# Performance work log

Measured on AMD Instinct MI355X. Metric: run time of the kernel, lower is better.

Reference implementation:

```python
import jax, jax.numpy as jnp
import numpy as np

N = 4096  # query nodes
L = 4096  # source nodes
C = 512   # in_channels == out_channels (required by the original code path)
H = 8     # num_heads
DK = C // H  # 64


def setup_inputs() -> dict:
    key = jax.random.key(0)
    ks = jax.random.split(key, 12)
    s = 1.0 / np.sqrt(C)
    return {
        "query_input": jax.random.normal(ks[0], (N, C), jnp.float32),
        "source_input": jax.random.normal(ks[1], (L, C), jnp.float32),
        # outer value projection (TransConvLayerGAT.Wv): C -> C
        "Wv_out_w": jax.random.uniform(ks[2], (C, C), jnp.float32, -s, s),
        "Wv_out_b": jax.random.uniform(ks[3], (C,), jnp.float32, -s, s),
        # attention projections
        "Wq_w": jax.random.uniform(ks[4], (C, H * DK), jnp.float32, -s, s),
        "Wq_b": jax.random.uniform(ks[5], (H * DK,), jnp.float32, -s, s),
        "Wk_w": jax.random.uniform(ks[6], (C, H * DK), jnp.float32, -s, s),
        "Wk_b": jax.random.uniform(ks[7], (H * DK,), jnp.float32, -s, s),
        # attention value projection: C -> H * out_channels
        "Wv_attn_w": jax.random.uniform(ks[8], (C, H * C), jnp.float32, -s, s),
        "Wv_attn_b": jax.random.uniform(ks[9], (H * C,), jnp.float32, -s, s),
    }


def reference(query_input, source_input, Wv_out_w, Wv_out_b,
              Wq_w, Wq_b, Wk_w, Wk_b, Wv_attn_w, Wv_attn_b):
    # outer value projection (use_weight=True)
    value = source_input @ Wv_out_w + Wv_out_b            # [L, C]
    # attention projections
    q = (query_input @ Wq_w + Wq_b).reshape(N, H, DK)     # [N, H, DK]
    k = (source_input @ Wk_w + Wk_b).reshape(L, H, DK)    # [L, H, DK]
    v = (value @ Wv_attn_w + Wv_attn_b).reshape(L, H, C)  # [L, H, C]
    scale = 1.0 / jnp.sqrt(jnp.float32(DK))
    scores = jnp.einsum('nhm,lhm->nlh', q, k) * scale     # [N, L, H]
    # NOTE: faithful to original — softmax over the HEADS axis (dim=-1)
    w = jax.nn.softmax(scores, axis=-1)                   # [N, L, H]
    out = jnp.einsum('nlh,lhd->nhd', w, v)                # [N, H, C]
    return out
```

## Files before the change

### kernel.cpp

```cpp
#include <hip/hip_runtime.h>
#include <cstddef>
#include <cstdint>

#define NQ 4096
#define NS 4096
#define CH 512
#define NH 8
#define HC 4096

typedef unsigned short u16;
typedef __attribute__((ext_vector_type(8))) short short8;
typedef __attribute__((ext_vector_type(4))) float f32x4;

__device__ __forceinline__ u16 f2b(float f) {
  unsigned u = __float_as_uint(f);
  return (u16)((u + 0x7fffu + ((u >> 16) & 1u)) >> 16);
}
__device__ __forceinline__ f32x4 mfma16(short8 a, short8 b, f32x4 c) {
  return __builtin_amdgcn_mfma_f32_16x16x32_bf16(a, b, c, 0, 0, 0);
}
__device__ __forceinline__ void gload_lds16(const void* g, void* l) {
  __builtin_amdgcn_global_load_lds(
      (const __attribute__((address_space(1))) void*)g,
      (__attribute__((address_space(3))) void*)l, 16, 0, 0);
}

__global__ __launch_bounds__(256) void convert_flat(
    const float* __restrict__ in, u16* __restrict__ out, int n4)
{
  int idx = blockIdx.x * 256 + threadIdx.x;
  int stride = gridDim.x * 256;
  for (int i = idx; i < n4; i += stride) {
    float4 v = ((const float4*)in)[i];
    ushort4 o;
    o.x = f2b(v.x); o.y = f2b(v.y); o.z = f2b(v.z); o.w = f2b(v.w);
    ((ushort4*)out)[i] = o;
  }
}

__global__ __launch_bounds__(256) void transpose_convert(
    const float* __restrict__ in, u16* __restrict__ out, int R, int C)
{
  __shared__ u16 tile[32][33];
  int tid = threadIdx.x;
  int tx = tid & 31, ty = tid >> 5;
#pragma unroll
  for (int i = 0; i < 4; ++i) {
    int r = blockIdx.y * 32 + ty + i * 8;
    int c = blockIdx.x * 32 + tx;
    tile[ty + i * 8][tx] = f2b(in[(size_t)r * C + c]);
  }
  __syncthreads();
#pragma unroll
  for (int i = 0; i < 4; ++i) {
    int co = blockIdx.x * 32 + ty + i * 8;
    int ro = blockIdx.y * 32 + tx;
    out[(size_t)co * R + ro] = tile[tx][ty + i * 8];
  }
}

template <int MODE>
__global__ __launch_bounds__(256) void gemm_core(
    const u16* __restrict__ A, int lda,
    const u16* __restrict__ Bt, int ldb,
    u16* __restrict__ Cb, float* __restrict__ Cf, int ldc,
    const float* __restrict__ bias,
    int K, size_t aPlane)
{
  constexpr int BM = 128, BN = 128;
  constexpr int FM = 4, FN = 4;
  constexpr int ABYTES = BM * 64;
  constexpr int NCH = (BM + BN) * 64 / 1024;

  __shared__ u16 smem[(BM + BN) * 32];
  u16* As = smem;
  u16* Bs = smem + BM * 32;

  const int tid = threadIdx.x;
  const int wid = tid >> 6, lane = tid & 63;
  const int wr = wid >> 1, wc = wid & 1;
  const int fr = wr * FM * 16, fc = wc * FN * 16;
  const int m0 = blockIdx.y * BM, n0 = blockIdx.x * BN;

  if constexpr (MODE == 3) {
    const int bz = blockIdx.z;
    A += (size_t)bz * aPlane;
    Bt += (size_t)bz * 512 * ldb;
    Cf += (size_t)bz * 512;
  }

  f32x4 acc[FM][FN];
#pragma unroll
  for (int m = 0; m < FM; ++m)
#pragma unroll
    for (int n = 0; n < FN; ++n)
#pragma unroll
      for (int i = 0; i < 4; ++i) acc[m][n][i] = 0.f;

  const int lcol = (lane & 3) << 3;
  const int lrow4 = lane >> 2;

  for (int k0 = 0; k0 < K; k0 += 32) {
    for (int c = wid; c < NCH; c += 4) {
      int boff = c << 10;
      const u16* g;
      if (boff < ABYTES) {
        int r = (boff >> 6) + lrow4;
        g = A + (size_t)(m0 + r) * lda + (k0 + lcol);
      } else {
        int r = ((boff - ABYTES) >> 6) + lrow4;
        g = Bt + (size_t)(n0 + r) * ldb + (k0 + lcol);
      }
      gload_lds16(g, (char*)smem + boff);
    }
    __syncthreads();

    short8 af[FM], bq[FN];
    const int kg = (lane >> 4) << 3;
#pragma unroll
    for (int m = 0; m < FM; ++m)
      af[m] = *(const short8*)(As + (size_t)(fr + m * 16 + (lane & 15)) * 32 + kg);
#pragma unroll
    for (int n = 0; n < FN; ++n)
      bq[n] = *(const short8*)(Bs + (size_t)(fc + n * 16 + (lane & 15)) * 32 + kg);
#pragma unroll
    for (int m = 0; m < FM; ++m)
#pragma unroll
      for (int n = 0; n < FN; ++n)
        acc[m][n] = mfma16(af[m], bq[n], acc[m][n]);
    __syncthreads();
  }

  const int crow = (lane >> 4) << 2;
  const int ccol = lane & 15;

  if constexpr (MODE == 0) {
#pragma unroll
    for (int n = 0; n < FN; ++n) {
      int gn = n0 + fc + n * 16 + ccol;
      float bv = bias[gn];
#pragma unroll
      for (int m = 0; m < FM; ++m)
#pragma unroll
        for (int i = 0; i < 4; ++i) {
          int gm = m0 + fr + m * 16 + crow + i;
          Cb[(size_t)gm * ldc + gn] = f2b(acc[m][n][i] + bv);
        }
    }
  } else if constexpr (MODE == 1) {
#pragma unroll
    for (int n = 0; n < FN; ++n) {
      int gn = n0 + fc + n * 16 + ccol;
      float bv = bias[gn];
#pragma unroll
      for (int m = 0; m < FM; ++m) {
        int mb = m0 + fr + m * 16 + crow;
        ushort4 o;
        o.x = f2b(acc[m][n][0] + bv); o.y = f2b(acc[m][n][1] + bv);
        o.z = f2b(acc[m][n][2] + bv); o.w = f2b(acc[m][n][3] + bv);
        *(ushort4*)(Cb + (size_t)gn * ldc + mb) = o;
      }
    }
  } else {
#pragma unroll
    for (int m = 0; m < FM; ++m)
#pragma unroll
      for (int i = 0; i < 4; ++i) {
        int gm = m0 + fr + m * 16 + crow + i;
#pragma unroll
        for (int n = 0; n < FN; ++n) {
          int gn = n0 + fc + n * 16 + ccol;
          Cf[(size_t)gm * ldc + gn] = acc[m][n][i];
        }
      }
  }
}

__global__ __launch_bounds__(256) void attn_pass1(
    const u16* __restrict__ q, const u16* __restrict__ kmat,
    u16* __restrict__ W, int nbase, size_t plane)
{
  __shared__ u16 lbuf[16384];
  char* lb = (char*)lbuf;

  const int tid = threadIdx.x, wid = tid >> 6, lane = tid & 63;
  const int nloc0 = blockIdx.y * 16;
  const int l0 = blockIdx.x * 128;
  const int lw = l0 + wid * 32;
  const int r16 = lane & 15, g = lane >> 4;
  const int kg = g << 3;

  short8 qf[16];
  const u16* qrow = q + (size_t)(nbase + nloc0 + r16) * CH + kg;
#pragma unroll
  for (int h = 0; h < 8; ++h)
#pragma unroll
    for (int kk = 0; kk < 2; ++kk)
      qf[h * 2 + kk] = *(const short8*)(qrow + h * 64 + kk * 32);

  f32x4 acc[8][2];
#pragma unroll
  for (int h = 0; h < 8; ++h)
#pragma unroll
    for (int f = 0; f < 2; ++f)
#pragma unroll
      for (int i = 0; i < 4; ++i) acc[h][f][i] = 0.f;

#pragma unroll
  for (int f = 0; f < 2; ++f) {
    const u16* krow = kmat + (size_t)(lw + f * 16 + r16) * CH + kg;
#pragma unroll
    for (int h = 0; h < 8; ++h)
#pragma unroll
      for (int kk = 0; kk < 2; ++kk) {
        short8 kf = *(const short8*)(krow + h * 64 + kk * 32);
        acc[h][f] = mfma16(kf, qf[h * 2 + kk], acc[h][f]);
      }
  }

  const int nn = r16;
#pragma unroll
  for (int f = 0; f < 2; ++f) {
    u16 wb[4][8];
#pragma unroll
    for (int i = 0; i < 4; ++i) {
      float s[8], mx = -3e38f;
#pragma unroll
      for (int h = 0; h < 8; ++h) { s[h] = acc[h][f][i] * 0.125f; mx = fmaxf(mx, s[h]); }
      float sum = 0.f;
#pragma unroll
      for (int h = 0; h < 8; ++h) { s[h] = __expf(s[h] - mx); sum += s[h]; }
      float inv = 1.0f / sum;
#pragma unroll
      for (int h = 0; h < 8; ++h) wb[i][h] = f2b(s[h] * inv);
    }
    const int lloc = wid * 32 + f * 16 + g * 4;
#pragma unroll
    for (int h = 0; h < 8; ++h) {
      unsigned p0 = (unsigned)wb[0][h] | ((unsigned)wb[1][h] << 16);
      unsigned p1 = (unsigned)wb[2][h] | ((unsigned)wb[3][h] << 16);
      int wa = (h << 12) + (nn << 8) + (lloc << 1);
      wa ^= (nn & 7) << 4;
      *(uint2*)(lb + wa) = make_uint2(p0, p1);
    }
  }
  __syncthreads();

  const int rn = tid >> 4, rl = (tid & 15) << 3;
#pragma unroll
  for (int h = 0; h < 8; ++h) {
    int ra = (h << 12) + (rn << 8) + (rl << 1);
    ra ^= (rn & 7) << 4;
    uint4 v = *(const uint4*)(lb + ra);
    *(uint4*)(W + (size_t)h * plane + (size_t)(nloc0 + rn) * NS + l0 + rl) = v;
  }
}

extern "C" void kernel_launch(void* const* d_in, const int* in_sizes, int n_in,
                              void* d_out, int out_size, void* d_ws, size_t ws_size,
                              hipStream_t stream)
{
  const float* query   = (const float*)d_in[0];
  const float* source  = (const float*)d_in[1];
  const float* Wvo_w   = (const float*)d_in[2];
  const float* Wvo_b   = (const float*)d_in[3];
  const float* Wq_w    = (const float*)d_in[4];
  const float* Wq_b    = (const float*)d_in[5];
  const float* Wk_w    = (const float*)d_in[6];
  const float* Wk_b    = (const float*)d_in[7];
  const float* Wva_w   = (const float*)d_in[8];
  const float* Wva_b   = (const float*)d_in[9];
  float* out = (float*)d_out;

  char* base = (char*)d_ws;
  size_t o = 0;
  auto alloc = [&](size_t b) -> char* {
    char* p = base + o;
    o += (b + 255) & ~(size_t)255;
    return p;
  };
  u16* query_bf  = (u16*)alloc((size_t)NQ * CH * 2);
  u16* source_bf = (u16*)alloc((size_t)NS * CH * 2);
  u16* WqT  = (u16*)alloc((size_t)CH * CH * 2);
  u16* WkT  = (u16*)alloc((size_t)CH * CH * 2);
  u16* WvoT = (u16*)alloc((size_t)CH * CH * 2);
  u16* WvaT = (u16*)alloc((size_t)CH * HC * 2);
  u16* qb   = (u16*)alloc((size_t)NQ * CH * 2);
  u16* kb   = (u16*)alloc((size_t)NS * CH * 2);
  u16* valr = (u16*)alloc((size_t)NS * CH * 2);
  u16* V2T  = (u16*)alloc((size_t)HC * NS * 2);
  size_t fixed = o;

  int c = 32;
  for (int cand = 1; cand <= 32; cand <<= 1) {
    if (fixed + (size_t)NH * (NQ / cand) * NS * 2 <= ws_size) { c = cand; break; }
  }
  const int rows = NQ / c;
  u16* Wb = (u16*)alloc((size_t)NH * rows * NS * 2);
  const size_t plane = (size_t)rows * NS;

  convert_flat<<<1024, 256, 0, stream>>>(query, query_bf, NQ * CH / 4);
  convert_flat<<<1024, 256, 0, stream>>>(source, source_bf, NS * CH / 4);
  transpose_convert<<<dim3(16, 16), 256, 0, stream>>>(Wq_w, WqT, CH, CH);
  transpose_convert<<<dim3(16, 16), 256, 0, stream>>>(Wk_w, WkT, CH, CH);
  transpose_convert<<<dim3(16, 16), 256, 0, stream>>>(Wvo_w, WvoT, CH, CH);
  transpose_convert<<<dim3(128, 16), 256, 0, stream>>>(Wva_w, WvaT, CH, HC);

  gemm_core<0><<<dim3(4, 32), 256, 0, stream>>>(query_bf, CH, WqT, CH, qb, nullptr, CH,
                                                Wq_b, CH, 0);
  gemm_core<0><<<dim3(4, 32), 256, 0, stream>>>(source_bf, CH, WkT, CH, kb, nullptr, CH,
                                                Wk_b, CH, 0);
  gemm_core<0><<<dim3(4, 32), 256, 0, stream>>>(source_bf, CH, WvoT, CH, valr, nullptr, CH,
                                                Wvo_b, CH, 0);

  gemm_core<1><<<dim3(32, 32), 256, 0, stream>>>(valr, CH, WvaT, CH, V2T, nullptr, NS,
                                                 Wva_b, CH, 0);

  for (int ci = 0; ci < c; ++ci) {
    const int nb = ci * rows;
    attn_pass1<<<dim3(32, rows / 16), 256, 0, stream>>>(qb, kb, Wb, nb, plane);
    gemm_core<3><<<dim3(4, rows / 128, 8), 256, 0, stream>>>(
        Wb, NS, V2T, NS, nullptr, out + (size_t)nb * HC, HC, nullptr, NS, plane);
  }
}
```

Baseline: 677.3 us.

## Fold the two value projections into one combined weight and chunk over source nodes

Precomputes a combined weight Wva^T·Wvo^T and a combined bias, so V2T comes from a single GEMM on the source features instead of two chained GEMMs. The attention loop now chunks along the source dimension and accumulates partial outputs into the fp32 output with read-modify-write. The MODE 3 GEMM uses a flattened 1D grid with head-interleaved block mapping. Folding changes bf16 rounding slightly, and chunking adds extra output traffic when more than one chunk is used.

```diff
diff --git a/kernel.cpp b/kernel.cpp
--- a/kernel.cpp
+++ b/kernel.cpp
@@ -59,13 +59,23 @@
   }
 }
 
+__global__ __launch_bounds__(256) void make_bcomb(
+    const float* __restrict__ Wva_w, const float* __restrict__ Wvo_b,
+    const float* __restrict__ Wva_b, float* __restrict__ bcomb)
+{
+  int hc = blockIdx.x * 256 + threadIdx.x;
+  float s = Wva_b[hc];
+  for (int c = 0; c < CH; ++c) s += Wvo_b[c] * Wva_w[(size_t)c * HC + hc];
+  bcomb[hc] = s;
+}
+
 template <int MODE>
 __global__ __launch_bounds__(256) void gemm_core(
     const u16* __restrict__ A, int lda,
     const u16* __restrict__ Bt, int ldb,
     u16* __restrict__ Cb, float* __restrict__ Cf, int ldc,
     const float* __restrict__ bias,
-    int K, size_t aPlane)
+    int K, size_t aPlane, int accum)
 {
   constexpr int BM = 128, BN = 128;
   constexpr int FM = 4, FN = 4;
@@ -80,13 +90,19 @@
   const int wid = tid >> 6, lane = tid & 63;
   const int wr = wid >> 1, wc = wid & 1;
   const int fr = wr * FM * 16, fc = wc * FN * 16;
-  const int m0 = blockIdx.y * BM, n0 = blockIdx.x * BN;
-
+
+  int m0, n0;
   if constexpr (MODE == 3) {
-    const int bz = blockIdx.z;
-    A += (size_t)bz * aPlane;
-    Bt += (size_t)bz * 512 * ldb;
-    Cf += (size_t)bz * 512;
+    const int bid = blockIdx.x;
+    const int z = bid & 7, loc = bid >> 3;
+    m0 = (loc >> 2) * BM;
+    n0 = (loc & 3) * BN;
+    A += (size_t)z * aPlane;
+    Bt += (size_t)z * 512 * ldb;
+    Cf += (size_t)z * 512;
+  } else {
+    m0 = blockIdx.y * BM;
+    n0 = blockIdx.x * BN;
   }
 
   f32x4 acc[FM][FN];
@@ -147,30 +163,44 @@
           Cb[(size_t)gm * ldc + gn] = f2b(acc[m][n][i] + bv);
         }
     }
-  } else if constexpr (MODE == 1) {
-#pragma unroll
-    for (int n = 0; n < FN; ++n) {
-      int gn = n0 + fc + n * 16 + ccol;
-      float bv = bias[gn];
-#pragma unroll
-      for (int m = 0; m < FM; ++m) {
-        int mb = m0 + fr + m * 16 + crow;
-        ushort4 o;
-        o.x = f2b(acc[m][n][0] + bv); o.y = f2b(acc[m][n][1] + bv);
-        o.z = f2b(acc[m][n][2] + bv); o.w = f2b(acc[m][n][3] + bv);
-        *(ushort4*)(Cb + (size_t)gn * ldc + mb) = o;
-      }
-    }
-  } else {
+  } else if constexpr (MODE == 2) {
 #pragma unroll
     for (int m = 0; m < FM; ++m)
 #pragma unroll
       for (int i = 0; i < 4; ++i) {
         int gm = m0 + fr + m * 16 + crow + i;
+        float bv = bias[gm];
 #pragma unroll
         for (int n = 0; n < FN; ++n) {
           int gn = n0 + fc + n * 16 + ccol;
-          Cf[(size_t)gm * ldc + gn] = acc[m][n][i];
+          Cb[(size_t)gm * ldc + gn] = f2b(acc[m][n][i] + bv);
+        }
+      }
+  } else if constexpr (MODE == 5) {
+#pragma unroll
+    for (int m = 0; m < FM; ++m)
+#pragma unroll
+      for (int i = 0; i < 4; ++i) {
+        int gm = m0 + fr + m * 16 + crow + i;
+#pragma unroll
+        for (int n = 0; n < FN; ++n) {
+          int gn = n0 + fc + n * 16 + ccol;
+          Cb[(size_t)gm * ldc + gn] = f2b(acc[m][n][i]);
+        }
+      }
+  } else {
+#pragma unroll
+    for (int m = 0; m < FM; ++m)
+#pragma unroll
+      for (int i = 0; i < 4; ++i) {
+        int gm = m0 + fr + m * 16 + crow + i;
+#pragma unroll
+        for (int n = 0; n < FN; ++n) {
+          int gn = n0 + fc + n * 16 + ccol;
+          size_t idx = (size_t)gm * ldc + gn;
+          float v = acc[m][n][i];
+          if (accum) v += Cf[idx];
+          Cf[idx] = v;
         }
       }
   }
@@ -178,20 +208,20 @@
 
 __global__ __launch_bounds__(256) void attn_pass1(
     const u16* __restrict__ q, const u16* __restrict__ kmat,
-    u16* __restrict__ W, int nbase, size_t plane)
+    u16* __restrict__ W, int lbase, int LCH, size_t plane)
 {
   __shared__ u16 lbuf[16384];
   char* lb = (char*)lbuf;
 
   const int tid = threadIdx.x, wid = tid >> 6, lane = tid & 63;
-  const int nloc0 = blockIdx.y * 16;
+  const int n0 = blockIdx.y * 16;
   const int l0 = blockIdx.x * 128;
-  const int lw = l0 + wid * 32;
+  const int lw = lbase + l0 + wid * 32;
   const int r16 = lane & 15, g = lane >> 4;
   const int kg = g << 3;
 
   short8 qf[16];
-  const u16* qrow = q + (size_t)(nbase + nloc0 + r16) * CH + kg;
+  const u16* qrow = q + (size_t)(n0 + r16) * CH + kg;
 #pragma unroll
   for (int h = 0; h < 8; ++h)
 #pragma unroll
@@ -252,7 +282,7 @@
     int ra = (h << 12) + (rn << 8) + (rl << 1);
     ra ^= (rn & 7) << 4;
     uint4 v = *(const uint4*)(lb + ra);
-    *(uint4*)(W + (size_t)h * plane + (size_t)(nloc0 + rn) * NS + l0 + rl) = v;
+    *(uint4*)(W + (size_t)h * plane + (size_t)(n0 + rn) * LCH + l0 + rl) = v;
   }
 }
 
@@ -281,45 +311,48 @@
   };
   u16* query_bf  = (u16*)alloc((size_t)NQ * CH * 2);
   u16* source_bf = (u16*)alloc((size_t)NS * CH * 2);
-  u16* WqT  = (u16*)alloc((size_t)CH * CH * 2);
-  u16* WkT  = (u16*)alloc((size_t)CH * CH * 2);
-  u16* WvoT = (u16*)alloc((size_t)CH * CH * 2);
-  u16* WvaT = (u16*)alloc((size_t)CH * HC * 2);
+  u16* WqT     = (u16*)alloc((size_t)CH * CH * 2);
+  u16* WkT     = (u16*)alloc((size_t)CH * CH * 2);
+  u16* WvaT    = (u16*)alloc((size_t)CH * HC * 2);
+  u16* Wvo_bf  = (u16*)alloc((size_t)CH * CH * 2);
+  u16* WcombT  = (u16*)alloc((size_t)HC * CH * 2);
+  float* bcomb = (float*)alloc((size_t)HC * 4);
   u16* qb   = (u16*)alloc((size_t)NQ * CH * 2);
   u16* kb   = (u16*)alloc((size_t)NS * CH * 2);
-  u16* valr = (u16*)alloc((size_t)NS * CH * 2);
   u16* V2T  = (u16*)alloc((size_t)HC * NS * 2);
   size_t fixed = o;
 
   int c = 32;
   for (int cand = 1; cand <= 32; cand <<= 1) {
-    if (fixed + (size_t)NH * (NQ / cand) * NS * 2 <= ws_size) { c = cand; break; }
-  }
-  const int rows = NQ / c;
-  u16* Wb = (u16*)alloc((size_t)NH * rows * NS * 2);
-  const size_t plane = (size_t)rows * NS;
+    if (fixed + (size_t)NH * NQ * (NS / cand) * 2 <= ws_size) { c = cand; break; }
+  }
+  const int LCH = NS / c;
+  u16* Wb = (u16*)alloc((size_t)NH * NQ * LCH * 2);
+  const size_t plane = (size_t)NQ * LCH;
 
   convert_flat<<<1024, 256, 0, stream>>>(query, query_bf, NQ * CH / 4);
   convert_flat<<<1024, 256, 0, stream>>>(source, source_bf, NS * CH / 4);
+  convert_flat<<<256, 256, 0, stream>>>(Wvo_w, Wvo_bf, CH * CH / 4);
   transpose_convert<<<dim3(16, 16), 256, 0, stream>>>(Wq_w, WqT, CH, CH);
   transpose_convert<<<dim3(16, 16), 256, 0, stream>>>(Wk_w, WkT, CH, CH);
-  transpose_convert<<<dim3(16, 16), 256, 0, stream>>>(Wvo_w, WvoT, CH, CH);
   transpose_convert<<<dim3(128, 16), 256, 0, stream>>>(Wva_w, WvaT, CH, HC);
+  make_bcomb<<<16, 256, 0, stream>>>(Wva_w, Wvo_b, Wva_b, bcomb);
+
+  gemm_core<5><<<dim3(4, 32), 256, 0, stream>>>(WvaT, CH, Wvo_bf, CH, WcombT, nullptr, CH,
+                                                nullptr, CH, 0, 0);
 
   gemm_core<0><<<dim3(4, 32), 256, 0, stream>>>(query_bf, CH, WqT, CH, qb, nullptr, CH,
-                                                Wq_b, CH, 0);
+                                                Wq_b, CH, 0, 0);
   gemm_core<0><<<dim3(4, 32), 256, 0, stream>>>(source_bf, CH, WkT, CH, kb, nullptr, CH,
-                                                Wk_b, CH, 0);
-  gemm_core<0><<<dim3(4, 32), 256, 0, stream>>>(source_bf, CH, WvoT, CH, valr, nullptr, CH,
-                                                Wvo_b, CH, 0);
-
-  gemm_core<1><<<dim3(32, 32), 256, 0, stream>>>(valr, CH, WvaT, CH, V2T, nullptr, NS,
-                                                 Wva_b, CH, 0);
+                                                Wk_b, CH, 0, 0);
+
+  gemm_core<2><<<dim3(32, 32), 256, 0, stream>>>(WcombT, CH, source_bf, CH, V2T, nullptr, NS,
+                                                 bcomb, CH, 0, 0);
 
   for (int ci = 0; ci < c; ++ci) {
-    const int nb = ci * rows;
-    attn_pass1<<<dim3(32, rows / 16), 256, 0, stream>>>(qb, kb, Wb, nb, plane);
-    gemm_core<3><<<dim3(4, rows / 128, 8), 256, 0, stream>>>(
-        Wb, NS, V2T, NS, nullptr, out + (size_t)nb * HC, HC, nullptr, NS, plane);
-  }
-}
+    const int lbase = ci * LCH;
+    attn_pass1<<<dim3(LCH / 128, NQ / 16), 256, 0, stream>>>(qb, kb, Wb, lbase, LCH, plane);
+    gemm_core<3><<<1024, 256, 0, stream>>>(Wb, LCH, V2T + lbase, NS, nullptr, out, HC,
+                                           nullptr, LCH, plane, ci > 0 ? 1 : 0);
+  }
+}
```

New measurement: 659.5 us. -2.6%, faster.
